# Kernel optimization log

Measured on AMD Instinct MI355X. Metric: run time of the kernel, lower is better.

## Reference

```python
import jax, jax.numpy as jnp
import numpy as np

N = 100000   # nodes
E = 1600000  # edges (avg degree 16)
H = 128      # hidden_dim
G = 256      # graphs in batch
IN = 2       # input feature dim (GCNConv(2, hidden_dim))


def setup_inputs() -> dict:
    key = jax.random.key(0)
    ks = jax.random.split(key, 12)
    def lin(k, fan_in, shape):
        # kaiming-uniform-ish init, scale irrelevant for correctness testing
        return jax.random.uniform(k, shape, jnp.float32, -1.0, 1.0) / np.sqrt(fan_in).astype(np.float32)
    return {
        "x": jax.random.normal(ks[0], (N, IN), jnp.float32),
        "edge_src": jax.random.randint(ks[1], (E,), 0, N, jnp.int32),
        "edge_dst": jax.random.randint(ks[2], (E,), 0, N, jnp.int32),
        "batch_ids": jnp.sort(jax.random.randint(ks[3], (N,), 0, G, jnp.int32)),
        "num_graphs": G,
        "W1": lin(ks[4], IN, (IN, H)), "b1": jnp.zeros((H,), jnp.float32),
        "W2": lin(ks[5], H, (H, H)),  "b2": jnp.zeros((H,), jnp.float32),
        "fc1_W": lin(ks[6], H, (H, H)), "fc1_b": lin(ks[7], H, (H,)),
        "fc2_W": lin(ks[8], H, (H, 1)), "fc2_b": lin(ks[9], H, (1,)),
    }


def gcn_layer(x, W, b, src, dst, n):
    # PyG GCNConv: add self-loops, symmetric deg^{-1/2} normalization,
    # linear transform, scatter-add aggregation, bias.
    h = x @ W                                                     # [N, H]
    deg = jax.ops.segment_sum(jnp.ones_like(src, jnp.float32), dst, num_segments=n) + 1.0  # +1 self-loop
    dinv = jax.lax.rsqrt(deg)                                     # [N]
    norm = dinv[src] * dinv[dst]                                  # [E]
    agg = jax.ops.segment_sum(h[src] * norm[:, None], dst, num_segments=n)  # [N, H]
    # self-loop contribution: deg_i^{-1/2} * deg_i^{-1/2} = 1/deg_i
    return agg + h * (1.0 / deg)[:, None] + b


def reference(x, edge_src, edge_dst, batch_ids, num_graphs,
              W1, b1, W2, b2, fc1_W, fc1_b, fc2_W, fc2_b):
    n = x.shape[0]
    h = jax.nn.relu(gcn_layer(x, W1, b1, edge_src, edge_dst, n))
    h = jax.nn.relu(gcn_layer(h, W2, b2, edge_src, edge_dst, n))
    # global_mean_pool
    sums = jax.ops.segment_sum(h, batch_ids, num_segments=num_graphs)            # [G, H]
    cnt = jax.ops.segment_sum(jnp.ones((n,), jnp.float32), batch_ids, num_segments=num_graphs)
    pooled = sums / jnp.maximum(cnt, 1.0)[:, None]
    h = jax.nn.relu(pooled @ fc1_W + fc1_b)
    return h @ fc2_W + fc2_b                                                     # [G, 1]
```

## Files before the change

### kernel.cpp

```cpp
#include <hip/hip_runtime.h>
#include <stdint.h>

#define HD 128
#define BSH 8
#define BNODES 256
#define PER 8
#define SCAP 256
#define BINBLK 256

typedef float f32x4 __attribute__((ext_vector_type(4)));
typedef float f32x2 __attribute__((ext_vector_type(2)));
typedef short s16x8 __attribute__((ext_vector_type(8)));

static inline int idiv(int a, int b) { return (a + b - 1) / b; }

__device__ __forceinline__ unsigned short f2b(float f) {
  unsigned u = __float_as_uint(f);
  return (unsigned short)((u + 0x7fffu + ((u >> 16) & 1u)) >> 16);
}

__global__ void __launch_bounds__(256) k_w2t_bincount(
    const float* __restrict__ W2, unsigned* __restrict__ w2f,
    float4* __restrict__ td, const int* __restrict__ edst,
    int* __restrict__ cntm, int E, int NB, int chunk, int N) {
  if (blockIdx.x < 8) {
    int f = blockIdx.x * 256 + threadIdx.x;
    if (f == 0) td[N] = make_float4(0.f, 0.f, 0.f, 0.f);
    if (f >= 2048) return;
    int c = f >> 8, s = (f >> 6) & 3, lane = f & 63;
    int col = c * 16 + (lane & 15);
    int kb = s * 32 + (lane >> 4) * 8;
    unsigned hi4[4], lo4[4];
#pragma unroll
    for (int j = 0; j < 4; ++j) {
      float w0 = W2[(kb + 2 * j) * HD + col];
      float w1 = W2[(kb + 2 * j + 1) * HD + col];
      unsigned short h0 = f2b(w0), h1 = f2b(w1);
      float r0 = w0 - __uint_as_float((unsigned)h0 << 16);
      float r1 = w1 - __uint_as_float((unsigned)h1 << 16);
      unsigned short l0 = f2b(r0), l1 = f2b(r1);
      hi4[j] = ((unsigned)h1 << 16) | h0;
      lo4[j] = ((unsigned)l1 << 16) | l0;
    }
    *(uint4*)&w2f[f * 4] = make_uint4(hi4[0], hi4[1], hi4[2], hi4[3]);
    *(uint4*)&w2f[8192 + f * 4] = make_uint4(lo4[0], lo4[1], lo4[2], lo4[3]);
    return;
  }
  __shared__ int hist[512];
  int blk = blockIdx.x - 8;
  for (int b = threadIdx.x; b < 512; b += 256) hist[b] = 0;
  __syncthreads();
  int s0 = blk * chunk, s1 = min(E, s0 + chunk);
  for (int k = s0 + threadIdx.x; k < s1; k += 256)
    atomicAdd(&hist[edst[k] >> BSH], 1);
  __syncthreads();
  for (int b = threadIdx.x; b < NB; b += 256)
    cntm[(size_t)b * BINBLK + blk] = hist[b];
}

__global__ void k_scan1(const int* __restrict__ cnt, int* __restrict__ part, int N) {
  __shared__ int sh[256];
  int t = threadIdx.x;
  int base = blockIdx.x * 1024 + t * 4;
  int s = 0;
#pragma unroll
  for (int u = 0; u < 4; ++u) { int idx = base + u; if (idx < N) s += cnt[idx]; }
  sh[t] = s; __syncthreads();
  for (int off = 128; off > 0; off >>= 1) { if (t < off) sh[t] += sh[t + off]; __syncthreads(); }
  if (t == 0) part[blockIdx.x] = sh[0];
}

__global__ void k_scan2(int* part, int nb) {
  __shared__ int sh[1024];
  int t = threadIdx.x;
  int v = (t < nb) ? part[t] : 0;
  sh[t] = v;
  __syncthreads();
  for (int off = 1; off < 1024; off <<= 1) {
    int add = (t >= off) ? sh[t - off] : 0;
    __syncthreads();
    sh[t] += add;
    __syncthreads();
  }
  if (t < nb) part[t] = sh[t] - v;
}

__global__ void k_scan3(const int* __restrict__ cnt, const int* __restrict__ part,
                        int* __restrict__ out, int N) {
  __shared__ int sa[256], sb[256];
  int t = threadIdx.x;
  int base = blockIdx.x * 1024 + t * 4;
  int v[4]; int s = 0;
#pragma unroll
  for (int u = 0; u < 4; ++u) { int idx = base + u; v[u] = (idx < N) ? cnt[idx] : 0; s += v[u]; }
  sa[t] = s; __syncthreads();
  int* cur = sa; int* nxt = sb;
  for (int off = 1; off < 256; off <<= 1) {
    int val = cur[t] + ((t >= off) ? cur[t - off] : 0);
    nxt[t] = val; __syncthreads();
    int* tmp = cur; cur = nxt; nxt = tmp;
  }
  int excl = cur[t] - s + part[blockIdx.x];
#pragma unroll
  for (int u = 0; u < 4; ++u) {
    int idx = base + u;
    if (idx < N) { out[idx] = excl; excl += v[u]; }
  }
}

__global__ void __launch_bounds__(256) k_binscatter(const int* __restrict__ esrc,
                                                    const int* __restrict__ edst,
                                                    const int* __restrict__ scanM,
                                                    unsigned* __restrict__ recs,
                                                    int E, int NB, int chunk) {
  __shared__ int cur[512];
  int blk = blockIdx.x;
  for (int b = threadIdx.x; b < NB; b += 256) cur[b] = scanM[(size_t)b * BINBLK + blk];
  __syncthreads();
  int s0 = blk * chunk, s1 = min(E, s0 + chunk);
  for (int k = s0 + threadIdx.x; k < s1; k += 256) {
    int d = edst[k], s = esrc[k];
    int b = d >> BSH;
    int pos = atomicAdd(&cur[b], 1);
    recs[pos] = ((unsigned)(d & (BNODES - 1)) << 23) | (unsigned)s;
  }
}

__global__ void __launch_bounds__(256) k_bucketsort(const unsigned* __restrict__ recs,
                                                    const int* __restrict__ scanM,
                                                    const float* __restrict__ x,
                                                    const int* __restrict__ bids,
                                                    unsigned* __restrict__ ssrc16,
                                                    int* __restrict__ row_start,
                                                    int* __restrict__ cnt,
                                                    float* __restrict__ dinv,
                                                    float2* __restrict__ xs,
                                                    int* __restrict__ gstart,
                                                    int NB, int N, int G, int E) {
  __shared__ int count[BNODES], excl[BNODES], cur[BNODES], psum[32];
  int b = blockIdx.x;
  int t = threadIdx.x;
  count[t] = 0;
  __syncthreads();
  int rs = scanM[(size_t)b * BINBLK];
  int re = (b == NB - 1) ? E : scanM[(size_t)(b + 1) * BINBLK];
  int base_p = rs + b * BNODES;
  for (int k = rs + t; k < re; k += 256) atomicAdd(&count[recs[k] >> 23], 1);
  __syncthreads();
  if (t < 32) {
    int s = 0;
#pragma unroll
    for (int u = 0; u < 8; ++u) s += (count[t * 8 + u] + 1) & ~1;
    psum[t] = s;
  }
  __syncthreads();
  if (t == 0) {
    int run = 0;
    for (int d = 0; d < 32; ++d) { int v = psum[d]; psum[d] = run; run += v; }
  }
  __syncthreads();
  if (t < 32) {
    int run = psum[t];
#pragma unroll
    for (int u = 0; u < 8; ++u) {
      excl[t * 8 + u] = run;
      run += (count[t * 8 + u] + 1) & ~1;
    }
  }
  __syncthreads();
  {
    int d = t;
    int i = b * BNODES + d;
    if (i < N) {
      cnt[i] = count[d];
      row_start[i] = base_p + excl[d];
      if (count[d] & 1)
        ssrc16[base_p + excl[d] + count[d]] = (unsigned)N << 4;
      float di = rsqrtf((float)(count[d] + 1));
      dinv[i] = di;
      float2 xv = *(const float2*)&x[2 * i];
      xs[i] = make_float2(di * xv.x, di * xv.y);
      int g = bids[i];
      if (i == 0)
        for (int gg = 0; gg <= g; ++gg) gstart[gg] = 0;
      int gn = (i == N - 1) ? G : bids[i + 1];
      for (int gg = g + 1; gg <= gn; ++gg) gstart[gg] = i + 1;
    }
    cur[d] = excl[d];
  }
  __syncthreads();
  for (int k = rs + t; k < re; k += 256) {
    unsigned r = recs[k];
    int dl = r >> 23;
    int pos = base_p + atomicAdd(&cur[dl], 1);
    ssrc16[pos] = (r & 0x007fffffu) << 4;
  }
}

__global__ void k_aggx2(const int* __restrict__ row_start, const int* __restrict__ cnt,
                        const unsigned* __restrict__ ssrc16, const float2* __restrict__ xs,
                        const float* __restrict__ dinv, float4* __restrict__ td, int N) {
  int i = blockIdx.x * 256 + threadIdx.x;
  if (i >= N) return;
  int rs = row_start[i], re = rs + cnt[i];
  float a0 = 0.f, a1 = 0.f, b0 = 0.f, b1 = 0.f;
  int k = rs;
  for (; k + 3 < re; k += 4) {
    unsigned v0 = ssrc16[k] >> 4, v1 = ssrc16[k + 1] >> 4;
    unsigned v2 = ssrc16[k + 2] >> 4, v3 = ssrc16[k + 3] >> 4;
    float2 p0 = xs[v0], p1 = xs[v1], p2 = xs[v2], p3 = xs[v3];
    a0 += p0.x + p1.x; a1 += p0.y + p1.y;
    b0 += p2.x + p3.x; b1 += p2.y + p3.y;
  }
  for (; k < re; ++k) {
    float2 p = xs[ssrc16[k] >> 4];
    a0 += p.x; a1 += p.y;
  }
  a0 += b0; a1 += b1;
  float2 self = xs[i];
  float di = dinv[i];
  td[i] = make_float4(di * (a0 + self.x), di * (a1 + self.y), di, 0.f);
}

__global__ void __launch_bounds__(256) k_aggh(
    const int* __restrict__ row_start, const int* __restrict__ cnt,
    const unsigned* __restrict__ ssrc16, const float4* __restrict__ td,
    const float* __restrict__ W1, const float* __restrict__ b1,
    unsigned* __restrict__ m_b, int N) {
  __shared__ float4 sbuf[4][SCAP];
  int wave = threadIdx.x >> 6;
  int lane = threadIdx.x & 63;
  int wid = blockIdx.x * 4 + wave;
  int i0 = wid * PER;
  if (i0 >= N) return;
  int nn = min(N - i0, PER);
  int hl = lane >> 5;
  int fq = (lane & 31) * 4;
  f32x4 w0 = *(const f32x4*)&W1[fq];
  f32x4 w1 = *(const f32x4*)&W1[HD + fq];
  f32x4 bb = *(const f32x4*)&b1[fq];
  int mydeg = (lane < nn) ? cnt[i0 + lane] : 0;
  int myrow = (lane < nn) ? row_start[i0 + lane] : 0;
  float4 mytd = (lane < nn) ? td[i0 + lane] : make_float4(0.f, 0.f, 0.f, 0.f);
  int mx = __float_as_int(mytd.x), my = __float_as_int(mytd.y), mz = __float_as_int(mytd.z);
  int rs0 = __builtin_amdgcn_readfirstlane(myrow);
  int last = nn - 1;
  int rsEnd = __builtin_amdgcn_readlane(myrow, last) +
              ((__builtin_amdgcn_readlane(mydeg, last) + 1) & ~1);
  int total = rsEnd - rs0;
  const char* tdc = (const char*)td;
  bool staged = (total <= SCAP);
  if (staged) {
#pragma unroll
    for (int w = 0; w < SCAP / 64; ++w) {
      int sl = w * 64 + lane;
      if (sl < total) {
        unsigned off = ssrc16[rs0 + sl];
        sbuf[wave][sl] = *(const float4*)(tdc + off);
      }
    }
  }
  int k = 0;
  const f32x4 zero4 = {0.f, 0.f, 0.f, 0.f};
#define EDGE_F(T, ACC) { \
    f32x4 h = f32x4{T.y, T.y, T.y, T.y} * w1 + bb; \
    h = f32x4{T.x, T.x, T.x, T.x} * w0 + h; \
    h = __builtin_elementwise_max(h, zero4); \
    ACC = f32x4{T.z, T.z, T.z, T.z} * h + ACC; }
  for (int node = 0; node < nn; ++node) {
    int deg = __builtin_amdgcn_readlane(mydeg, node);
    int np = (deg + 1) >> 1;
    f32x4 acc = zero4, acc2 = zero4;
    if (staged) {
      const float4* buf = &sbuf[wave][k + hl];
      int p = 0;
      for (; p + 1 < np; p += 2) {
        float4 t0 = buf[2 * p];
        float4 t1 = buf[2 * p + 2];
        EDGE_F(t0, acc)
        EDGE_F(t1, acc2)
      }
      if (p < np) {
        float4 t0 = buf[2 * p];
        EDGE_F(t0, acc)
      }
    } else {
      for (int p = 0; p < np; ++p) {
        unsigned off = ssrc16[rs0 + k + 2 * p + hl];
        float4 t = *(const float4*)(tdc + off);
        EDGE_F(t, acc)
      }
    }
    k += np * 2;
#pragma unroll
    for (int c = 0; c < 4; ++c) acc[c] += acc2[c];
    f32x4 tot;
#pragma unroll
    for (int c = 0; c < 4; ++c) tot[c] = acc[c] + __shfl_xor(acc[c], 32);
    float tx = __int_as_float(__builtin_amdgcn_readlane(mx, node));
    float ty = __int_as_float(__builtin_amdgcn_readlane(my, node));
    float tz = __int_as_float(__builtin_amdgcn_readlane(mz, node));
    f32x4 h = f32x4{ty, ty, ty, ty} * w1 + bb;
    h = f32x4{tx, tx, tx, tx} * w0 + h;
    h = __builtin_elementwise_max(h, zero4);
    f32x4 r = f32x4{tz, tz, tz, tz} * h + tot;
    float v0 = (hl ? r[2] : r[0]) * tz;
    float v1 = (hl ? r[3] : r[1]) * tz;
    int j = hl ? (2 * (lane - 32) + 1) : (2 * lane);
    m_b[(unsigned)(i0 + node) * 64 + j] = ((unsigned)f2b(v1) << 16) | f2b(v0);
  }
#undef EDGE_F
}

__global__ void __launch_bounds__(256) k_t2pool(
    const unsigned* __restrict__ m_b, const unsigned* __restrict__ w2f,
    const float* __restrict__ b2, const int* __restrict__ gstart,
    const float* __restrict__ fc1W, const float* __restrict__ fc1b,
    const float* __restrict__ fc2W, const float* __restrict__ fc2b,
    float* __restrict__ out, int N, int G) {
  __shared__ unsigned W[16384];
  __shared__ float pool[16][HD];
  __shared__ float ps[HD];
  __shared__ float rsh[HD];
  int g = blockIdx.x;
  for (int u = threadIdx.x; u < 4096; u += 256)
    *(uint4*)&W[u * 4] = *(const uint4*)&w2f[u * 4];
  for (int u = threadIdx.x; u < 16 * HD; u += 256) ((float*)pool)[u] = 0.f;
  const int lane = threadIdx.x & 63;
  const int wave = threadIdx.x >> 6;
  const int col = lane & 15;
  const int kg = lane >> 4;
  float bb[8];
#pragma unroll
  for (int c = 0; c < 8; ++c) bb[c] = b2[c * 16 + col];
  int s0 = gstart[g], e0 = gstart[g + 1];
  int ntiles = (e0 - s0 + 15) >> 4;
  float pacc[8];
#pragma unroll
  for (int c = 0; c < 8; ++c) pacc[c] = 0.f;
  __syncthreads();
  for (int tile = wave; tile < ntiles; tile += 4) {
    int rbase = s0 + tile * 16;
    int arow = rbase + col;
    if (arow >= N) arow = N - 1;
    f32x4 acc[8];
#pragma unroll
    for (int c = 0; c < 8; ++c) acc[c] = f32x4{0.f, 0.f, 0.f, 0.f};
#pragma unroll
    for (int s = 0; s < 4; ++s) {
      uint4 av = *(const uint4*)&m_b[((size_t)arow << 6) + s * 16 + kg * 4];
      s16x8 A = *(s16x8*)&av;
#pragma unroll
      for (int c = 0; c < 8; ++c) {
        int f = (c * 4 + s) * 64 + lane;
        s16x8 Bh = *(s16x8*)&W[f * 4];
        s16x8 Bl = *(s16x8*)&W[8192 + f * 4];
        acc[c] = __builtin_amdgcn_mfma_f32_16x16x32_bf16(A, Bh, acc[c], 0, 0, 0);
        acc[c] = __builtin_amdgcn_mfma_f32_16x16x32_bf16(A, Bl, acc[c], 0, 0, 0);
      }
    }
    int orow = rbase + kg * 4;
#pragma unroll
    for (int c = 0; c < 8; ++c) {
#pragma unroll
      for (int r = 0; r < 4; ++r) {
        if (orow + r < e0) pacc[c] += fmaxf(acc[c][r] + bb[c], 0.f);
      }
    }
  }
#pragma unroll
  for (int c = 0; c < 8; ++c) pool[wave * 4 + kg][c * 16 + col] = pacc[c];
  __syncthreads();
  int j = threadIdx.x;
  if (j < HD) {
    float a = 0.f;
#pragma unroll
    for (int r = 0; r < 16; ++r) a += pool[r][j];
    float cg = (float)(e0 - s0);
    cg = cg < 1.f ? 1.f : cg;
    ps[j] = a / cg;
  }
  __syncthreads();
  if (j < HD) {
    float a = fc1b[j];
#pragma unroll 4
    for (int k = 0; k < HD; ++k) a = fmaf(ps[k], fc1W[k * HD + j], a);
    rsh[j] = fmaxf(a, 0.f) * fc2W[j];
  }
  __syncthreads();
  for (int off = 64; off > 0; off >>= 1) {
    if (j < off) rsh[j] += rsh[j + off];
    __syncthreads();
  }
  if (j == 0) out[g] = rsh[0] + fc2b[0];
}

extern "C" void kernel_launch(void* const* d_in, const int* in_sizes, int n_in,
                              void* d_out, int out_size, void* d_ws, size_t ws_size,
                              hipStream_t stream) {
  const float* x    = (const float*)d_in[0];
  const int* esrc   = (const int*)d_in[1];
  const int* edst   = (const int*)d_in[2];
  const int* bids   = (const int*)d_in[3];
  const float* W1   = (const float*)d_in[5];
  const float* b1   = (const float*)d_in[6];
  const float* W2   = (const float*)d_in[7];
  const float* b2   = (const float*)d_in[8];
  const float* fc1W = (const float*)d_in[9];
  const float* fc1b = (const float*)d_in[10];
  const float* fc2W = (const float*)d_in[11];
  const float* fc2b = (const float*)d_in[12];
  float* out = (float*)d_out;

  const int N = in_sizes[0] / 2;
  const int E = in_sizes[1];
  const int G = out_size;

  const int NB = idiv(N, BNODES);
  const int M = NB * BINBLK;
  const int chunk = idiv(E, BINBLK);

  char* w = (char*)d_ws;
  size_t o = 0;
  auto take = [&](size_t b) -> char* {
    char* p = w + o;
    o = (o + b + 255) & ~(size_t)255;
    return p;
  };
  int*      cntm      = (int*)     take((size_t)M * 4);
  int*      scanM     = (int*)     take((size_t)M * 4);
  int*      part      = (int*)     take(4096);
  unsigned* recs      = (unsigned*)take((size_t)E * 4);
  unsigned* ssrc16    = (unsigned*)take((size_t)(E + N + 256) * 4);
  int*      cnt       = (int*)     take((size_t)N * 4);
  int*      row_start = (int*)     take((size_t)N * 4);
  float*    dinv      = (float*)   take((size_t)N * 4);
  float*    xs        = (float*)   take((size_t)N * 8);
  float*    td        = (float*)   take((size_t)(N + 1) * 16);
  int*      gstart    = (int*)     take((size_t)(G + 1) * 4);
  unsigned* m_b       = (unsigned*)take((size_t)N * 64 * 4);
  unsigned* w2f       = (unsigned*)take(16384 * 4);

  int nbM = idiv(M, 1024);
  k_w2t_bincount<<<8 + BINBLK, 256, 0, stream>>>(W2, w2f, (float4*)td, edst,
                                                 cntm, E, NB, chunk, N);
  k_scan1<<<nbM, 256, 0, stream>>>(cntm, part, M);
  k_scan2<<<1, 1024, 0, stream>>>(part, nbM);
  k_scan3<<<nbM, 256, 0, stream>>>(cntm, part, scanM, M);
  k_binscatter<<<BINBLK, 256, 0, stream>>>(esrc, edst, scanM, recs, E, NB, chunk);
  k_bucketsort<<<NB, 256, 0, stream>>>(recs, scanM, x, bids, ssrc16, row_start,
                                       cnt, dinv, (float2*)xs, gstart, NB, N, G, E);
  k_aggx2<<<idiv(N, 256), 256, 0, stream>>>(row_start, cnt, ssrc16, (const float2*)xs,
                                            dinv, (float4*)td, N);
  int waves = idiv(N, PER);
  k_aggh<<<idiv(waves, 4), 256, 0, stream>>>(row_start, cnt, ssrc16, (const float4*)td,
                                             W1, b1, m_b, N);
  k_t2pool<<<G, 256, 0, stream>>>(m_b, w2f, b2, gstart, fc1W, fc1b, fc2W, fc2b, out, N, G);
}
```

Baseline: 122.1 us.

## Split layer-1 aggregation wave into four edge groups with 8 features per lane

The layer-1 aggregation kernel now processes four edges in parallel per wave (16 lanes each, 8 features per lane) instead of two edge halves with 4 features per lane. Edge lists are padded to multiples of four with a dummy zero node, and the padded buffer is enlarged to match. Each node's output is written as one 16-byte store from a quarter of the wave, replacing per-lane 4-byte stores. This is meant to halve the number of per-edge loop iterations for the serial degree walk, at the cost of more padding work, an extra shuffle stage in the reduction, and higher register use.

```diff
diff --git a/kernel.cpp b/kernel.cpp
--- a/kernel.cpp
+++ b/kernel.cpp
@@ -9,7 +9,6 @@
 #define BINBLK 256
 
 typedef float f32x4 __attribute__((ext_vector_type(4)));
-typedef float f32x2 __attribute__((ext_vector_type(2)));
 typedef short s16x8 __attribute__((ext_vector_type(8)));
 
 static inline int idiv(int a, int b) { return (a + b - 1) / b; }
@@ -144,13 +143,13 @@
   __syncthreads();
   int rs = scanM[(size_t)b * BINBLK];
   int re = (b == NB - 1) ? E : scanM[(size_t)(b + 1) * BINBLK];
-  int base_p = rs + b * BNODES;
+  int base_p = rs + b * 3 * BNODES;
   for (int k = rs + t; k < re; k += 256) atomicAdd(&count[recs[k] >> 23], 1);
   __syncthreads();
   if (t < 32) {
     int s = 0;
 #pragma unroll
-    for (int u = 0; u < 8; ++u) s += (count[t * 8 + u] + 1) & ~1;
+    for (int u = 0; u < 8; ++u) s += (count[t * 8 + u] + 3) & ~3;
     psum[t] = s;
   }
   __syncthreads();
@@ -164,7 +163,7 @@
 #pragma unroll
     for (int u = 0; u < 8; ++u) {
       excl[t * 8 + u] = run;
-      run += (count[t * 8 + u] + 1) & ~1;
+      run += (count[t * 8 + u] + 3) & ~3;
     }
   }
   __syncthreads();
@@ -174,8 +173,9 @@
     if (i < N) {
       cnt[i] = count[d];
       row_start[i] = base_p + excl[d];
-      if (count[d] & 1)
-        ssrc16[base_p + excl[d] + count[d]] = (unsigned)N << 4;
+      int pad = (count[d] + 3) & ~3;
+      for (int pp = count[d]; pp < pad; ++pp)
+        ssrc16[base_p + excl[d] + pp] = (unsigned)N << 4;
       float di = rsqrtf((float)(count[d] + 1));
       dinv[i] = di;
       float2 xv = *(const float2*)&x[2 * i];
@@ -234,11 +234,12 @@
   int i0 = wid * PER;
   if (i0 >= N) return;
   int nn = min(N - i0, PER);
-  int hl = lane >> 5;
-  int fq = (lane & 31) * 4;
-  f32x4 w0 = *(const f32x4*)&W1[fq];
-  f32x4 w1 = *(const f32x4*)&W1[HD + fq];
-  f32x4 bb = *(const f32x4*)&b1[fq];
+  int qg = lane >> 4;
+  int sl = lane & 15;
+  int fb = sl * 8;
+  f32x4 w0a = *(const f32x4*)&W1[fb],      w0b = *(const f32x4*)&W1[fb + 4];
+  f32x4 w1a = *(const f32x4*)&W1[HD + fb], w1b = *(const f32x4*)&W1[HD + fb + 4];
+  f32x4 bba = *(const f32x4*)&b1[fb],      bbb = *(const f32x4*)&b1[fb + 4];
   int mydeg = (lane < nn) ? cnt[i0 + lane] : 0;
   int myrow = (lane < nn) ? row_start[i0 + lane] : 0;
   float4 mytd = (lane < nn) ? td[i0 + lane] : make_float4(0.f, 0.f, 0.f, 0.f);
@@ -246,70 +247,87 @@
   int rs0 = __builtin_amdgcn_readfirstlane(myrow);
   int last = nn - 1;
   int rsEnd = __builtin_amdgcn_readlane(myrow, last) +
-              ((__builtin_amdgcn_readlane(mydeg, last) + 1) & ~1);
+              ((__builtin_amdgcn_readlane(mydeg, last) + 3) & ~3);
   int total = rsEnd - rs0;
   const char* tdc = (const char*)td;
   bool staged = (total <= SCAP);
   if (staged) {
 #pragma unroll
     for (int w = 0; w < SCAP / 64; ++w) {
-      int sl = w * 64 + lane;
-      if (sl < total) {
-        unsigned off = ssrc16[rs0 + sl];
-        sbuf[wave][sl] = *(const float4*)(tdc + off);
+      int sl2 = w * 64 + lane;
+      if (sl2 < total) {
+        unsigned off = ssrc16[rs0 + sl2];
+        sbuf[wave][sl2] = *(const float4*)(tdc + off);
       }
     }
   }
   int k = 0;
   const f32x4 zero4 = {0.f, 0.f, 0.f, 0.f};
-#define EDGE_F(T, ACC) { \
-    f32x4 h = f32x4{T.y, T.y, T.y, T.y} * w1 + bb; \
-    h = f32x4{T.x, T.x, T.x, T.x} * w0 + h; \
-    h = __builtin_elementwise_max(h, zero4); \
-    ACC = f32x4{T.z, T.z, T.z, T.z} * h + ACC; }
+#define EDGE_Q(T, A, B) { \
+    f32x4 ha = f32x4{T.y, T.y, T.y, T.y} * w1a + bba; \
+    f32x4 hb = f32x4{T.y, T.y, T.y, T.y} * w1b + bbb; \
+    ha = f32x4{T.x, T.x, T.x, T.x} * w0a + ha; \
+    hb = f32x4{T.x, T.x, T.x, T.x} * w0b + hb; \
+    ha = __builtin_elementwise_max(ha, zero4); \
+    hb = __builtin_elementwise_max(hb, zero4); \
+    A = f32x4{T.z, T.z, T.z, T.z} * ha + A; \
+    B = f32x4{T.z, T.z, T.z, T.z} * hb + B; }
   for (int node = 0; node < nn; ++node) {
     int deg = __builtin_amdgcn_readlane(mydeg, node);
-    int np = (deg + 1) >> 1;
-    f32x4 acc = zero4, acc2 = zero4;
+    int nq = (deg + 3) >> 2;
+    f32x4 aA = zero4, aB = zero4, cA = zero4, cB = zero4;
     if (staged) {
-      const float4* buf = &sbuf[wave][k + hl];
-      int p = 0;
-      for (; p + 1 < np; p += 2) {
-        float4 t0 = buf[2 * p];
-        float4 t1 = buf[2 * p + 2];
-        EDGE_F(t0, acc)
-        EDGE_F(t1, acc2)
-      }
-      if (p < np) {
-        float4 t0 = buf[2 * p];
-        EDGE_F(t0, acc)
+      const float4* buf = &sbuf[wave][k + qg];
+      int q = 0;
+      for (; q + 1 < nq; q += 2) {
+        float4 t0 = buf[4 * q];
+        float4 t1 = buf[4 * q + 4];
+        EDGE_Q(t0, aA, aB)
+        EDGE_Q(t1, cA, cB)
+      }
+      if (q < nq) {
+        float4 t0 = buf[4 * q];
+        EDGE_Q(t0, aA, aB)
       }
     } else {
-      for (int p = 0; p < np; ++p) {
-        unsigned off = ssrc16[rs0 + k + 2 * p + hl];
+      for (int q = 0; q < nq; ++q) {
+        unsigned off = ssrc16[rs0 + k + 4 * q + qg];
         float4 t = *(const float4*)(tdc + off);
-        EDGE_F(t, acc)
-      }
-    }
-    k += np * 2;
-#pragma unroll
-    for (int c = 0; c < 4; ++c) acc[c] += acc2[c];
-    f32x4 tot;
-#pragma unroll
-    for (int c = 0; c < 4; ++c) tot[c] = acc[c] + __shfl_xor(acc[c], 32);
+        EDGE_Q(t, aA, aB)
+      }
+    }
+    k += nq * 4;
+#pragma unroll
+    for (int c = 0; c < 4; ++c) { aA[c] += cA[c]; aB[c] += cB[c]; }
+    f32x4 tA, tB;
+#pragma unroll
+    for (int c = 0; c < 4; ++c) {
+      float v = aA[c] + __shfl_xor(aA[c], 16);
+      tA[c] = v + __shfl_xor(v, 32);
+      float u = aB[c] + __shfl_xor(aB[c], 16);
+      tB[c] = u + __shfl_xor(u, 32);
+    }
     float tx = __int_as_float(__builtin_amdgcn_readlane(mx, node));
     float ty = __int_as_float(__builtin_amdgcn_readlane(my, node));
     float tz = __int_as_float(__builtin_amdgcn_readlane(mz, node));
-    f32x4 h = f32x4{ty, ty, ty, ty} * w1 + bb;
-    h = f32x4{tx, tx, tx, tx} * w0 + h;
-    h = __builtin_elementwise_max(h, zero4);
-    f32x4 r = f32x4{tz, tz, tz, tz} * h + tot;
-    float v0 = (hl ? r[2] : r[0]) * tz;
-    float v1 = (hl ? r[3] : r[1]) * tz;
-    int j = hl ? (2 * (lane - 32) + 1) : (2 * lane);
-    m_b[(unsigned)(i0 + node) * 64 + j] = ((unsigned)f2b(v1) << 16) | f2b(v0);
-  }
-#undef EDGE_F
+    f32x4 ha = f32x4{ty, ty, ty, ty} * w1a + bba;
+    f32x4 hb = f32x4{ty, ty, ty, ty} * w1b + bbb;
+    ha = f32x4{tx, tx, tx, tx} * w0a + ha;
+    hb = f32x4{tx, tx, tx, tx} * w0b + hb;
+    ha = __builtin_elementwise_max(ha, zero4);
+    hb = __builtin_elementwise_max(hb, zero4);
+    f32x4 rA = f32x4{tz, tz, tz, tz} * ha + tA;
+    f32x4 rB = f32x4{tz, tz, tz, tz} * hb + tB;
+    if (qg == 0) {
+      uint4 o;
+      o.x = ((unsigned)f2b(tz * rA[1]) << 16) | f2b(tz * rA[0]);
+      o.y = ((unsigned)f2b(tz * rA[3]) << 16) | f2b(tz * rA[2]);
+      o.z = ((unsigned)f2b(tz * rB[1]) << 16) | f2b(tz * rB[0]);
+      o.w = ((unsigned)f2b(tz * rB[3]) << 16) | f2b(tz * rB[2]);
+      *(uint4*)&m_b[(unsigned)(i0 + node) * 64 + sl * 4] = o;
+    }
+  }
+#undef EDGE_Q
 }
 
 __global__ void __launch_bounds__(256) k_t2pool(
@@ -431,7 +449,7 @@
   int*      scanM     = (int*)     take((size_t)M * 4);
   int*      part      = (int*)     take(4096);
   unsigned* recs      = (unsigned*)take((size_t)E * 4);
-  unsigned* ssrc16    = (unsigned*)take((size_t)(E + N + 256) * 4);
+  unsigned* ssrc16    = (unsigned*)take((size_t)(E + 3 * (size_t)N + 512) * 4);
   int*      cnt       = (int*)     take((size_t)N * 4);
   int*      row_start = (int*)     take((size_t)N * 4);
   float*    dinv      = (float*)   take((size_t)N * 4);
```

Result: slower. 132.1 us (median of 2 runs) (+8.2%).
